# Kernel optimization log

Hardware: AMD Instinct MI355X
Metric: run time of the kernel (lower is better)

## Reference

```python
import jax, jax.numpy as jnp
import numpy as np

N = 4096   # support size
B = 512    # number of histograms (columns)


def setup_inputs() -> dict:
    key = jax.random.key(0)
    kU, kP, kK = jax.random.split(key, 3)
    # u must satisfy u < lamda; uniform [0,1) with lamda=10 is safe.
    U = jax.random.uniform(kU, (N, B), dtype=jnp.float32)
    # strictly positive histograms (avoid log(0))
    P = jax.random.uniform(kP, (N, B), dtype=jnp.float32) + 0.01
    # positive Gibbs kernel
    K = jax.random.uniform(kK, (N, N), dtype=jnp.float32) + 1e-3
    return {"U": U, "P": P, "K": K, "eps": 1, "lamda": 10}


def reference(U, P, K, eps, lamda):
    """Vectorized OTModel.OT_unbal: sum over columns of the primal unbalanced OT
    value reconstructed from dual potential U.  gamma_ij = a_i * K_ij * f_j is
    never materialized; all reductions over gamma are contracted analytically.
    """
    eps = jnp.float32(eps)
    lamda = jnp.float32(lamda)
    # f in log domain: (lamda/eps) * log(lamda/(lamda-u))          [N, B]
    flog = (lamda / eps) * jnp.log(lamda / (lamda - U))
    f = jnp.exp(flog)
    # alpha/eps with the mean-scale stabilization from get_alpha_unbal
    scale = flog.mean(axis=0)                                      # [B]
    KF_stab = K @ jnp.exp(flog - scale)                            # [N, B]
    alpha_over_eps = jnp.log(P) - (jnp.log(KF_stab) + scale)       # [N, B]
    a = jnp.exp(alpha_over_eps)                                    # exp(alpha/eps)
    Kf = K @ f                                                     # [N, B]
    # (gamma @ flog).sum() = sum_i a_i * (K @ (f * flog))_i
    term1 = jnp.sum(a * (K @ (f * flog)))
    # (gamma.T @ (alpha/eps)).sum() = sum_i a_i * (alpha/eps)_i * (K @ f)_i
    term2 = jnp.sum(a * alpha_over_eps * Kf)
    # gamma.sum()
    term3 = jnp.sum(a * Kf)
    # gamma.sum(0)_j = f_j * (K^T @ a)_j
    gcol = f * (K.T @ a)                                           # [N, B]
    # q from get_q_unbal (unstabilized, as in the original)
    q = (lamda / (lamda - U)) ** (lamda / eps + 1.0) * (K.T @ (P / Kf))
    # KL(a,b) = sum(a*log(a/b) - a)   (inputs strictly positive here)
    kl = jnp.sum(gcol * jnp.log(gcol / q) - gcol)
    return eps * (term1 + term2 - term3) + lamda * kl
```

## Files before the change

kernel.cpp:

```cpp
#include <hip/hip_runtime.h>

#define NN 4096
#define BB 512

typedef __attribute__((ext_vector_type(4))) float f32x4;
typedef __attribute__((ext_vector_type(2))) long long2v;
typedef unsigned short ushort;
typedef unsigned char uchar;
typedef unsigned int uint;
typedef __attribute__((ext_vector_type(4))) ushort ushort4v;

#define ASCALE 16384.0f
#define AINV   6.103515625e-05f

__device__ __forceinline__ float scal_val(const void* p) {
    int b = *(const int*)p;
    if (b >= 1 && b <= 1000000) return (float)b;
    return __int_as_float(b);
}

__device__ __forceinline__ ushort f2bf(float x) {
    unsigned u = __float_as_uint(x);
    u += 0x7fffu + ((u >> 16) & 1u);
    return (ushort)(u >> 16);
}
__device__ __forceinline__ float bf2f(ushort b) {
    return __uint_as_float((uint)b << 16);
}

__device__ __forceinline__ uint pack4_fp8(float a, float b, float c, float d) {
    int v = __builtin_amdgcn_cvt_pk_fp8_f32(a, b, 0, false);
    v = __builtin_amdgcn_cvt_pk_fp8_f32(c, d, v, true);
    return (uint)v;
}

__device__ __forceinline__ void gload16(const void* g, void* l) {
    __builtin_amdgcn_global_load_lds(
        (const __attribute__((address_space(1))) unsigned int*)g,
        (__attribute__((address_space(3))) unsigned int*)l, 16, 0, 0);
}

__device__ __forceinline__ double wave_sum(double v) {
#pragma unroll
    for (int s = 32; s > 0; s >>= 1) v += __shfl_down(v, s, 64);
    return v;
}

__device__ __forceinline__ int kperm(int kk) {
    int c = kk >> 3;
    return (c & 3) * 16 + (c >> 2) * 8 + (kk & 7);
}


__global__ __launch_bounds__(256) void k_prep(const float* __restrict__ K,
                                              const float* __restrict__ U,
                                              uchar* __restrict__ Kb,
                                              uchar* __restrict__ KTb,
                                              uchar* __restrict__ fT,
                                              const void* epsp, const void* lamp) {
    __shared__ float tile[64][65];
    const int t = threadIdx.x;
    const int tx = t & 15, ty = t >> 4;
    const int bid = blockIdx.x;
    const int pp = kperm(tx * 4);

    if (bid < 4096) {
        const int c0 = (bid & 63) * 64, r0 = (bid >> 6) * 64;
#pragma unroll
        for (int it = 0; it < 4; ++it) {
            int row = ty + it * 16;
            float4 v = *(const float4*)&K[(size_t)(r0 + row) * NN + c0 + tx * 4];
            *(uint*)&Kb[(size_t)(r0 + row) * NN + c0 + pp] =
                pack4_fp8(v.x, v.y, v.z, v.w);
            tile[row][tx * 4 + 0] = v.x;
            tile[row][tx * 4 + 1] = v.y;
            tile[row][tx * 4 + 2] = v.z;
            tile[row][tx * 4 + 3] = v.w;
        }
        __syncthreads();
#pragma unroll
        for (int it = 0; it < 4; ++it) {
            int row = ty + it * 16;
            *(uint*)&KTb[(size_t)(c0 + row) * NN + r0 + pp] =
                pack4_fp8(tile[tx * 4 + 0][row], tile[tx * 4 + 1][row],
                          tile[tx * 4 + 2][row], tile[tx * 4 + 3][row]);
        }
    } else {
        const int r = bid - 4096;
        const int c0 = (r & 7) * 64;
        const int r0 = (r >> 3) * 64;
        const float eps = scal_val(epsp), lam = scal_val(lamp);
        const float rr = lam / eps;
#pragma unroll
        for (int it = 0; it < 4; ++it) {
            int row = ty + it * 16;
            float4 v = *(const float4*)&U[(size_t)(r0 + row) * BB + c0 + tx * 4];
            float uu[4] = {v.x, v.y, v.z, v.w};
#pragma unroll
            for (int k = 0; k < 4; ++k) {
                float L = __logf(lam / (lam - uu[k]));
                tile[row][tx * 4 + k] = __expf(rr * L);
            }
        }
        __syncthreads();
#pragma unroll
        for (int it = 0; it < 4; ++it) {
            int row = ty + it * 16;
            *(uint*)&fT[(size_t)(c0 + row) * NN + r0 + pp] =
                pack4_fp8(tile[tx * 4 + 0][row], tile[tx * 4 + 1][row],
                          tile[tx * 4 + 2][row], tile[tx * 4 + 3][row]);
        }
    }
}

__global__ __launch_bounds__(256) void k_gemm1(const uchar* __restrict__ Kb,
                                               const uchar* __restrict__ fT,
                                               ushort* __restrict__ Y1b) {
    __shared__ __align__(16) uchar As[2][128 * 64];
    __shared__ __align__(16) uchar Bf[2][64 * 64];

    const int tid = threadIdx.x;
    const int lane = tid & 63;
    const int w = tid >> 6;
    const int wm = w & 1, wn = w >> 1;
    const int bid = blockIdx.x;
    const int kh = bid & 3;
    const int i0 = ((bid >> 2) & 31) * 128;
    const int j0 = (bid >> 7) * 64;
    const int quad = lane >> 4;
    const int l15 = lane & 15;
    const int sw = (l15 >> 1) & 3;

    f32x4 zero = {0.f, 0.f, 0.f, 0.f};
    f32x4 acc[4][2];
#pragma unroll
    for (int mt = 0; mt < 4; ++mt)
#pragma unroll
        for (int nt = 0; nt < 2; ++nt) acc[mt][nt] = zero;

    const int rl = lane >> 2;
    const int goff = ((lane & 3) ^ ((lane >> 3) & 3)) * 16;

    auto stage = [&](int k0, int b) {
#pragma unroll
        for (int it = 0; it < 2; ++it) {
            const int rbase = w * 32 + it * 16;
            gload16(Kb + (size_t)(i0 + rbase + rl) * NN + k0 + goff,
                    &As[b][rbase * 64]);
        }
        gload16(fT + (size_t)(j0 + w * 16 + rl) * NN + k0 + goff,
                &Bf[b][(w * 16) * 64]);
    };

    const int kbase = kh * (NN / 4);
    stage(kbase, 0);
    __syncthreads();
    const int uoff = ((quad ^ sw) << 4);
    for (int step = 0; step < NN / 256; ++step) {
        const int cur = step & 1;
        if (step < NN / 256 - 1) stage(kbase + (step + 1) * 64, cur ^ 1);
        long2v av[4], bv[2];
#pragma unroll
        for (int mt = 0; mt < 4; ++mt)
            av[mt] = *(const long2v*)&As[cur][(wm * 64 + mt * 16 + l15) * 64 + uoff];
#pragma unroll
        for (int nt = 0; nt < 2; ++nt)
            bv[nt] = *(const long2v*)&Bf[cur][(wn * 32 + nt * 16 + l15) * 64 + uoff];
#pragma unroll
        for (int mt = 0; mt < 4; ++mt)
#pragma unroll
            for (int nt = 0; nt < 2; ++nt) {
                acc[mt][nt] = __builtin_amdgcn_mfma_f32_16x16x32_fp8_fp8(
                    av[mt].x, bv[nt].x, acc[mt][nt], 0, 0, 0);
                acc[mt][nt] = __builtin_amdgcn_mfma_f32_16x16x32_fp8_fp8(
                    av[mt].y, bv[nt].y, acc[mt][nt], 0, 0, 0);
            }
        __syncthreads();
    }

    ushort* o1 = Y1b + (size_t)kh * NN * BB;
#pragma unroll
    for (int mt = 0; mt < 4; ++mt)
#pragma unroll
        for (int nt = 0; nt < 2; ++nt) {
            const int ib = i0 + wm * 64 + mt * 16 + quad * 4;
            const int j = j0 + wn * 32 + nt * 16 + l15;
#pragma unroll
            for (int r = 0; r < 4; ++r)
                o1[(size_t)(ib + r) * BB + j] = f2bf(acc[mt][nt][r]);
        }
}

__global__ __launch_bounds__(256) void k_epi(const ushort* __restrict__ Y1b,
                                             const float* __restrict__ P,
                                             uchar* __restrict__ aT,
                                             double* __restrict__ parts) {
    __shared__ float ta[64][65];
    __shared__ double bred[4][2];
    const int t = threadIdx.x;
    const int lane = t & 63;
    const int w = t >> 6;
    const int tx = t & 15, ty = t >> 4;
    const int j0 = blockIdx.x * 64;
    const int i0 = blockIdx.y * 64;
    const int bid = blockIdx.y * 8 + blockIdx.x;
    const size_t H = (size_t)NN * BB;
    const int pp = kperm(tx * 4);

    double t2 = 0.0, t3 = 0.0;
#pragma unroll
    for (int it = 0; it < 4; ++it) {
        int row = ty + it * 16;
        size_t off = (size_t)(i0 + row) * BB + j0 + tx * 4;
        ushort4v q0 = *(const ushort4v*)(Y1b + off);
        ushort4v q1 = *(const ushort4v*)(Y1b + H + off);
        ushort4v q2 = *(const ushort4v*)(Y1b + 2 * H + off);
        ushort4v q3 = *(const ushort4v*)(Y1b + 3 * H + off);
        float4 p4 = *(const float4*)(P + off);
        float pv[4] = {p4.x, p4.y, p4.z, p4.w};
#pragma unroll
        for (int e = 0; e < 4; ++e) {
            float y1 = bf2f(q0[e]) + bf2f(q1[e]) + bf2f(q2[e]) + bf2f(q3[e]);
            float aij = pv[e] / y1;
            t2 += (double)(pv[e] * __logf(aij));
            t3 += (double)pv[e];
            ta[row][tx * 4 + e] = aij * ASCALE;
        }
    }
    __syncthreads();
#pragma unroll
    for (int it = 0; it < 4; ++it) {
        int row = ty + it * 16;
        *(uint*)&aT[(size_t)(j0 + row) * NN + i0 + pp] =
            pack4_fp8(ta[tx * 4 + 0][row], ta[tx * 4 + 1][row],
                      ta[tx * 4 + 2][row], ta[tx * 4 + 3][row]);
    }

    t2 = wave_sum(t2); t3 = wave_sum(t3);
    if (lane == 0) { bred[w][0] = t2; bred[w][1] = t3; }
    __syncthreads();
    if (t == 0) {
        double b = 0, c = 0;
#pragma unroll
        for (int ww = 0; ww < 4; ++ww) { b += bred[ww][0]; c += bred[ww][1]; }
        parts[2048 + bid] = b;
        parts[2560 + bid] = c;
    }
}

__global__ __launch_bounds__(256) void k_gemm2(const uchar* __restrict__ KTb,
                                               const uchar* __restrict__ aT,
                                               const float* __restrict__ U,
                                               const void* epsp, const void* lamp,
                                               double* __restrict__ parts) {
    __shared__ __align__(16) uchar As[2][128 * 64];
    __shared__ __align__(16) uchar Bs[2][64 * 64];
    __shared__ double bred[4][2];

    const float eps = scal_val(epsp), lam = scal_val(lamp);
    const float rr = lam / eps;
    const int tid = threadIdx.x;
    const int lane = tid & 63;
    const int w = tid >> 6;
    const int wm = w & 1, wn = w >> 1;
    const int bid = blockIdx.x;
    const int kh = bid & 3;
    const int i0 = ((bid >> 2) & 31) * 128;
    const int j0 = (bid >> 7) * 64;
    const int quad = lane >> 4;
    const int l15 = lane & 15;
    const int sw = (l15 >> 1) & 3;

    f32x4 zero = {0.f, 0.f, 0.f, 0.f};
    f32x4 acc[4][2];
#pragma unroll
    for (int mt = 0; mt < 4; ++mt)
#pragma unroll
        for (int nt = 0; nt < 2; ++nt) acc[mt][nt] = zero;

    const int rl = lane >> 2;
    const int goff = ((lane & 3) ^ ((lane >> 3) & 3)) * 16;

    auto stage = [&](int k0, int b) {
#pragma unroll
        for (int it = 0; it < 2; ++it) {
            const int rbase = w * 32 + it * 16;
            gload16(KTb + (size_t)(i0 + rbase + rl) * NN + k0 + goff,
                    &As[b][rbase * 64]);
        }
        gload16(aT + (size_t)(j0 + w * 16 + rl) * NN + k0 + goff,
                &Bs[b][(w * 16) * 64]);
    };

    const int kbase = kh * (NN / 4);
    stage(kbase, 0);
    __syncthreads();
    const int uoff = ((quad ^ sw) << 4);
    for (int step = 0; step < NN / 256; ++step) {
        const int cur = step & 1;
        if (step < NN / 256 - 1) stage(kbase + (step + 1) * 64, cur ^ 1);
        long2v av[4], bv[2];
#pragma unroll
        for (int mt = 0; mt < 4; ++mt)
            av[mt] = *(const long2v*)&As[cur][(wm * 64 + mt * 16 + l15) * 64 + uoff];
#pragma unroll
        for (int nt = 0; nt < 2; ++nt)
            bv[nt] = *(const long2v*)&Bs[cur][(wn * 32 + nt * 16 + l15) * 64 + uoff];
#pragma unroll
        for (int mt = 0; mt < 4; ++mt)
#pragma unroll
            for (int nt = 0; nt < 2; ++nt) {
                acc[mt][nt] = __builtin_amdgcn_mfma_f32_16x16x32_fp8_fp8(
                    av[mt].x, bv[nt].x, acc[mt][nt], 0, 0, 0);
                acc[mt][nt] = __builtin_amdgcn_mfma_f32_16x16x32_fp8_fp8(
                    av[mt].y, bv[nt].y, acc[mt][nt], 0, 0, 0);
            }
        __syncthreads();
    }

    double t1p = 0.0, klp = 0.0;
#pragma unroll
    for (int mt = 0; mt < 4; ++mt)
#pragma unroll
        for (int nt = 0; nt < 2; ++nt) {
            const int ib = i0 + wm * 64 + mt * 16 + quad * 4;
            const int j = j0 + wn * 32 + nt * 16 + l15;
#pragma unroll
            for (int r = 0; r < 4; ++r) {
                float s = acc[mt][nt][r] * AINV;
                float u = U[(size_t)(ib + r) * BB + j];
                float L = __logf(lam / (lam - u));
                float fv = __expf(rr * L);
                t1p += (double)(fv * rr * L * s);
                klp -= (double)(fv * (1.0f + L) * s);
            }
        }

    t1p = wave_sum(t1p); klp = wave_sum(klp);
    if (lane == 0) { bred[w][0] = t1p; bred[w][1] = klp; }
    __syncthreads();
    if (tid == 0) {
        double a = 0, b = 0;
#pragma unroll
        for (int ww = 0; ww < 4; ++ww) { a += bred[ww][0]; b += bred[ww][1]; }
        parts[bid] = a;
        parts[1024 + bid] = b;
    }
}

__global__ __launch_bounds__(256) void k_final(const double* __restrict__ parts,
                                               const void* epsp, const void* lamp,
                                               float* __restrict__ out) {
    __shared__ double red[4][4];
    const int tid = threadIdx.x;
    const int lane = tid & 63, w = tid >> 6;
    double s0 = 0.0, s1 = 0.0, s2 = 0.0, s3 = 0.0;
    for (int i = tid; i < 1024; i += 256) {
        s0 += parts[i];
        s1 += parts[1024 + i];
    }
    for (int i = tid; i < 512; i += 256) {
        s2 += parts[2048 + i];
        s3 += parts[2560 + i];
    }
    s0 = wave_sum(s0); s1 = wave_sum(s1); s2 = wave_sum(s2); s3 = wave_sum(s3);
    if (lane == 0) { red[w][0] = s0; red[w][1] = s1; red[w][2] = s2; red[w][3] = s3; }
    __syncthreads();
    if (tid == 0) {
        double t1 = 0, kl = 0, t2 = 0, t3 = 0;
#pragma unroll
        for (int ww = 0; ww < 4; ++ww) {
            t1 += red[ww][0]; kl += red[ww][1]; t2 += red[ww][2]; t3 += red[ww][3];
        }
        float eps = scal_val(epsp), lam = scal_val(lamp);
        out[0] = (float)((double)eps * (t1 + t2 - t3) + (double)lam * kl);
    }
}

extern "C" void kernel_launch(void* const* d_in, const int* in_sizes, int n_in,
                              void* d_out, int out_size, void* d_ws, size_t ws_size,
                              hipStream_t stream) {
    const float* U = (const float*)d_in[0];
    const float* P = (const float*)d_in[1];
    const float* K = (const float*)d_in[2];
    const void* epsp = d_in[3];
    const void* lamp = d_in[4];

    double* parts = (double*)d_ws;
    char* base = (char*)d_ws + (64 << 10);
    uchar* Kb   = (uchar*)base;
    uchar* KTb  = (uchar*)(base + ((size_t)16 << 20));
    uchar* fT   = (uchar*)(base + ((size_t)32 << 20));
    uchar* aT   = (uchar*)(base + ((size_t)34 << 20));
    ushort* Y1b = (ushort*)(base + ((size_t)36 << 20));

    k_prep<<<4608, 256, 0, stream>>>(K, U, Kb, KTb, fT, epsp, lamp);
    k_gemm1<<<1024, 256, 0, stream>>>(Kb, fT, Y1b);
    k_epi<<<dim3(8, 64), 256, 0, stream>>>(Y1b, P, aT, parts);
    k_gemm2<<<1024, 256, 0, stream>>>(KTb, aT, U, epsp, lamp, parts);
    k_final<<<1, 256, 0, stream>>>(parts, epsp, lamp, (float*)d_out);
}
```

Baseline: 169.1 us.

## Store FP8 GEMM operands in pre-tiled, pre-swizzled block layout for contiguous loads

The prep and scaling kernels now write the FP8 copies of K, K^T, f^T and a^T in a blocked layout. Each 128x64 or 64x64 k-tile is contiguous and already carries the LDS bank swizzle. The GEMM staging code then issues fully contiguous 1KB global-to-LDS loads per wave instead of strided row segments. The aim is better memory coalescing and simpler address arithmetic, at the cost of more complex scattered writes in the producer kernels.

```diff
diff --git a/kernel.cpp b/kernel.cpp
--- a/kernel.cpp
+++ b/kernel.cpp
@@ -50,6 +50,10 @@
     int c = kk >> 3;
     return (c & 3) * 16 + (c >> 2) * 8 + (kk & 7);
 }
+__device__ __forceinline__ int bpos(int row, int pp) {
+    return (((pp >> 4) ^ ((row >> 1) & 3)) << 4) | (pp & 15);
+}
+
 
 
 __global__ __launch_bounds__(256) void k_prep(const float* __restrict__ K,
@@ -70,8 +74,10 @@
         for (int it = 0; it < 4; ++it) {
             int row = ty + it * 16;
             float4 v = *(const float4*)&K[(size_t)(r0 + row) * NN + c0 + tx * 4];
-            *(uint*)&Kb[(size_t)(r0 + row) * NN + c0 + pp] =
-                pack4_fp8(v.x, v.y, v.z, v.w);
+            int i = r0 + row;
+            int off = (((i >> 7) * 64 + (c0 >> 6)) << 13) + (i & 127) * 64 +
+                      bpos(row, pp);
+            *(uint*)&Kb[off] = pack4_fp8(v.x, v.y, v.z, v.w);
             tile[row][tx * 4 + 0] = v.x;
             tile[row][tx * 4 + 1] = v.y;
             tile[row][tx * 4 + 2] = v.z;
@@ -81,7 +87,10 @@
 #pragma unroll
         for (int it = 0; it < 4; ++it) {
             int row = ty + it * 16;
-            *(uint*)&KTb[(size_t)(c0 + row) * NN + r0 + pp] =
+            int i = c0 + row;
+            int off = (((i >> 7) * 64 + (r0 >> 6)) << 13) + (i & 127) * 64 +
+                      bpos(row, pp);
+            *(uint*)&KTb[off] =
                 pack4_fp8(tile[tx * 4 + 0][row], tile[tx * 4 + 1][row],
                           tile[tx * 4 + 2][row], tile[tx * 4 + 3][row]);
         }
@@ -106,7 +115,10 @@
 #pragma unroll
         for (int it = 0; it < 4; ++it) {
             int row = ty + it * 16;
-            *(uint*)&fT[(size_t)(c0 + row) * NN + r0 + pp] =
+            int j = c0 + row;
+            int off = (((j >> 6) * 64 + (r0 >> 6)) << 12) + (j & 63) * 64 +
+                      bpos(row, pp);
+            *(uint*)&fT[off] =
                 pack4_fp8(tile[tx * 4 + 0][row], tile[tx * 4 + 1][row],
                           tile[tx * 4 + 2][row], tile[tx * 4 + 3][row]);
         }
@@ -138,27 +150,24 @@
 #pragma unroll
         for (int nt = 0; nt < 2; ++nt) acc[mt][nt] = zero;
 
-    const int rl = lane >> 2;
-    const int goff = ((lane & 3) ^ ((lane >> 3) & 3)) * 16;
-
-    auto stage = [&](int k0, int b) {
-#pragma unroll
-        for (int it = 0; it < 2; ++it) {
-            const int rbase = w * 32 + it * 16;
-            gload16(Kb + (size_t)(i0 + rbase + rl) * NN + k0 + goff,
-                    &As[b][rbase * 64]);
-        }
-        gload16(fT + (size_t)(j0 + w * 16 + rl) * NN + k0 + goff,
-                &Bf[b][(w * 16) * 64]);
+    const uchar* apanel = Kb + ((size_t)(i0 >> 7) << 19);
+    const uchar* bpanel = fT + ((size_t)(j0 >> 6) << 18);
+
+    auto stage = [&](int ks, int b) {
+        const uchar* ga = apanel + ((size_t)ks << 13) + w * 2048 + lane * 16;
+        gload16(ga, &As[b][w * 2048]);
+        gload16(ga + 1024, &As[b][w * 2048 + 1024]);
+        const uchar* gb = bpanel + ((size_t)ks << 12) + w * 1024 + lane * 16;
+        gload16(gb, &Bf[b][w * 1024]);
     };
 
-    const int kbase = kh * (NN / 4);
-    stage(kbase, 0);
+    const int ks0 = kh * 16;
+    stage(ks0, 0);
     __syncthreads();
     const int uoff = ((quad ^ sw) << 4);
-    for (int step = 0; step < NN / 256; ++step) {
+    for (int step = 0; step < 16; ++step) {
         const int cur = step & 1;
-        if (step < NN / 256 - 1) stage(kbase + (step + 1) * 64, cur ^ 1);
+        if (step < 15) stage(ks0 + step + 1, cur ^ 1);
         long2v av[4], bv[2];
 #pragma unroll
         for (int mt = 0; mt < 4; ++mt)
@@ -231,7 +240,10 @@
 #pragma unroll
     for (int it = 0; it < 4; ++it) {
         int row = ty + it * 16;
-        *(uint*)&aT[(size_t)(j0 + row) * NN + i0 + pp] =
+        int j = j0 + row;
+        int off = (((j >> 6) * 64 + (i0 >> 6)) << 12) + (j & 63) * 64 +
+                  bpos(row, pp);
+        *(uint*)&aT[off] =
             pack4_fp8(ta[tx * 4 + 0][row], ta[tx * 4 + 1][row],
                       ta[tx * 4 + 2][row], ta[tx * 4 + 3][row]);
     }
@@ -278,27 +290,24 @@
 #pragma unroll
         for (int nt = 0; nt < 2; ++nt) acc[mt][nt] = zero;
 
-    const int rl = lane >> 2;
-    const int goff = ((lane & 3) ^ ((lane >> 3) & 3)) * 16;
-
-    auto stage = [&](int k0, int b) {
-#pragma unroll
-        for (int it = 0; it < 2; ++it) {
-            const int rbase = w * 32 + it * 16;
-            gload16(KTb + (size_t)(i0 + rbase + rl) * NN + k0 + goff,
-                    &As[b][rbase * 64]);
-        }
-        gload16(aT + (size_t)(j0 + w * 16 + rl) * NN + k0 + goff,
-                &Bs[b][(w * 16) * 64]);
+    const uchar* apanel = KTb + ((size_t)(i0 >> 7) << 19);
+    const uchar* bpanel = aT + ((size_t)(j0 >> 6) << 18);
+
+    auto stage = [&](int ks, int b) {
+        const uchar* ga = apanel + ((size_t)ks << 13) + w * 2048 + lane * 16;
+        gload16(ga, &As[b][w * 2048]);
+        gload16(ga + 1024, &As[b][w * 2048 + 1024]);
+        const uchar* gb = bpanel + ((size_t)ks << 12) + w * 1024 + lane * 16;
+        gload16(gb, &Bs[b][w * 1024]);
     };
 
-    const int kbase = kh * (NN / 4);
-    stage(kbase, 0);
+    const int ks0 = kh * 16;
+    stage(ks0, 0);
     __syncthreads();
     const int uoff = ((quad ^ sw) << 4);
-    for (int step = 0; step < NN / 256; ++step) {
+    for (int step = 0; step < 16; ++step) {
         const int cur = step & 1;
-        if (step < NN / 256 - 1) stage(kbase + (step + 1) * 64, cur ^ 1);
+        if (step < 15) stage(ks0 + step + 1, cur ^ 1);
         long2v av[4], bv[2];
 #pragma unroll
         for (int mt = 0; mt < 4; ++mt)
```

New measurement: 164.6 us. 2.6% less time.
